# Optimization experiments

Measured on AMD Instinct MI355X. Metric: run time of the kernel, lower is better.

## Reference

```python
import jax, jax.numpy as jnp
import numpy as np

D = 128      # memory_dim
L = 64       # segment_len
SCALE = 1.0 / np.sqrt(D)
LN_EPS = 1e-5


def _layernorm(x, g, b):
    mu = x.mean(-1, keepdims=True)
    var = ((x - mu) ** 2).mean(-1, keepdims=True)
    return (x - mu) * jax.lax.rsqrt(var + LN_EPS) * g + b


def setup_inputs() -> dict:
    key = jax.random.key(0)
    ks = jax.random.split(key, 8)
    B, T, Hd = 4, 4096, 2048
    w = 0.02  # init scale for weight matrices
    return {
        "H": jax.random.normal(ks[0], (B, T, Hd), jnp.float32),
        "M": jax.random.normal(ks[1], (B, D, D), jnp.float32),  # [B,K=128,D=128]
        "ln_g": jnp.ones((Hd,), jnp.float32),
        "ln_b": jnp.zeros((Hd,), jnp.float32),
        "W_eta_w": jax.random.normal(ks[2], (Hd,), jnp.float32) * w,
        "W_eta_b": jnp.full((1,), -5.0, jnp.float32),
        "sum_q": jax.random.normal(ks[3], (D,), jnp.float32),
        "sp_w": jax.random.normal(ks[4], (Hd, D), jnp.float32) * w,
        "sp_b": jnp.zeros((D,), jnp.float32),
        "eta_ch": jnp.ones((D,), jnp.float32),
        "temp": jnp.ones((1,), jnp.float32),
        "W_qkv": jax.random.normal(ks[5], (Hd, 3 * D), jnp.float32) * w,
    }


def reference(H, M, ln_g, ln_b, W_eta_w, W_eta_b, sum_q, sp_w, sp_b, eta_ch, temp, W_qkv):
    B, T, _ = H.shape
    K = M.shape[1]
    S = T // L  # T chosen divisible by segment_len (no-pad branch)

    Hn = _layernorm(H, ln_g, ln_b)                      # [B,T,Hd]

    # ---- write_memory ----
    H_mem = Hn @ sp_w + sp_b                            # [B,T,D]
    eta_tokens = jnp.einsum('bth,h->bt', Hn, W_eta_w) + W_eta_b  # [B,T]

    H_segs = H_mem.reshape(B, S, L, D)
    summary_scores = jnp.einsum('d,bsld->bsl', sum_q, H_segs) * SCALE
    summary_w = jax.nn.softmax(summary_scores, axis=-1)
    Z_seg = jnp.einsum('bsl,bsld->bsd', summary_w, H_segs)       # [B,S,D]

    eta_sig = jax.nn.sigmoid(eta_tokens)                          # [B,T]
    eta_seg = eta_sig.reshape(B, S, L).max(axis=-1)[..., None]    # [B,S,1]

    scores = jnp.einsum('bsd,bkd->bsk', Z_seg, M) * SCALE * jnp.exp(temp)
    A = jax.nn.softmax(scores, axis=-1)                           # [B,S,K]
    DeltaM = jnp.einsum('bsk,bsd->bkd', A, Z_seg * eta_seg)       # [B,K,D]

    eta_avg = eta_seg.mean(axis=1, keepdims=True)                 # [B,1,1]
    gate = eta_avg * jax.nn.sigmoid(eta_ch)                       # [B,1,D]
    M_new = (1.0 - gate) * M + DeltaM / S

    norm_sq = jnp.sum(DeltaM ** 2) / S
    # diversity loss on M_new
    Mn = M_new / jnp.maximum(jnp.linalg.norm(M_new, axis=-1, keepdims=True), 1e-12)
    sim = jnp.einsum('bkd,bjd->bkj', Mn, Mn) * (1.0 - jnp.eye(K, dtype=M.dtype))
    div_loss = jnp.mean(sim ** 2)
    loss = norm_sq * 0.01 + div_loss * 0.1

    # ---- read_memory (from updated memory; K<=1024 -> dense softmax path) ----
    Q_r = Hn @ W_qkv[:, 2 * D:]                                   # [B,T,D]
    r_scores = jnp.einsum('btd,bkd->btk', Q_r, M_new)
    A_r = jax.nn.softmax(r_scores * 2.0, axis=-1)
    C = jnp.einsum('btk,bkd->btd', A_r, M_new)                    # [B,T,D]

    return C, loss
```

## Files before the change

kernel.cpp:

```cpp
#include <hip/hip_runtime.h>
#include <hip/hip_bf16.h>
#include <math.h>

#define HD   2048
#define DD   128
#define TT   4096
#define BB   4
#define MT   (BB*TT)
#define LSEG 64
#define SSEG 64
#define NCOL 256
#define SCALE_D 0.088388347648318447f

typedef _Float16 half8 __attribute__((ext_vector_type(8)));
typedef _Float16 half4v __attribute__((ext_vector_type(4)));
typedef float    f32x4 __attribute__((ext_vector_type(4)));

__device__ __forceinline__ float sigmf(float x){ return 1.f/(1.f+__expf(-x)); }

__device__ __forceinline__ void glds16(const void* g, void* l) {
  __builtin_amdgcn_global_load_lds(
      (const __attribute__((address_space(1))) unsigned int*)g,
      (__attribute__((address_space(3))) unsigned int*)l, 16, 0, 0);
}

__global__ void k_pre(const float* __restrict__ ln_g, const float* __restrict__ ln_b,
                      const float* __restrict__ sp_w, const float* __restrict__ sp_b,
                      const float* __restrict__ W_qkv, const float* __restrict__ W_eta_w,
                      const float* __restrict__ W_eta_b,
                      _Float16* __restrict__ Bp, float* __restrict__ s_vec,
                      float* __restrict__ cb_vec, float* __restrict__ we2,
                      float* __restrict__ scal)
{
  __shared__ float red1[256], red2[256];
  int n = blockIdx.x, t = threadIdx.x;
  float sp = 0.f, cp = 0.f;
  if (n < NCOL) {
    for (int h = t; h < HD; h += 256) {
      float w = (n < DD) ? sp_w[(size_t)h*DD + n] : W_qkv[(size_t)h*384 + 256 + (n-DD)];
      float g = ln_g[h], b = ln_b[h];
      Bp[(size_t)n*HD + h] = (_Float16)(g*w);
      sp += g*w; cp += b*w;
    }
  } else {
    for (int h = t; h < HD; h += 256) {
      float w = W_eta_w[h];
      float g = ln_g[h], b = ln_b[h];
      we2[h] = g*w;
      sp += g*w; cp += b*w;
    }
  }
  red1[t] = sp; red2[t] = cp;
  __syncthreads();
  for (int o = 128; o > 0; o >>= 1) {
    if (t < o) { red1[t] += red1[t+o]; red2[t] += red2[t+o]; }
    __syncthreads();
  }
  if (t == 0) {
    if (n < NCOL) {
      s_vec[n]  = red1[0];
      cb_vec[n] = red2[0] + ((n < DD) ? sp_b[n] : 0.f);
    } else {
      scal[0] = red1[0];
      scal[1] = red2[0] + W_eta_b[0];
      scal[2] = 0.f; scal[3] = 0.f;
    }
  }
}

__launch_bounds__(512, 2)
__global__ void k01(const float* __restrict__ H, const _Float16* __restrict__ Bp,
                    const float* __restrict__ we2,
                    float* __restrict__ Cp, float* __restrict__ Sp)
{
  __shared__ __align__(16) char pool[133120];
  __shared__ float we_s[1024];
  _Float16* sA  = (_Float16*)pool;
  _Float16* sB  = (_Float16*)(pool + 32768);
  float*    sHm = (float*)pool;

  int tid = threadIdx.x;
  int mt = blockIdx.x & 127, kh = blockIdx.x >> 7;
  int m0r = mt * 128;
  int w = tid >> 6, lane = tid & 63;
  int wr = w >> 2, wc = w & 3;
  int fcol = lane & 15, kq = lane >> 4;

  if (tid < 256)
    ((float4*)we_s)[tid] = ((const float4*)(we2 + kh*1024))[tid];
  __syncthreads();

  int r_l = tid >> 2, s4 = tid & 3;
  const float* aptr = H + (size_t)(m0r + r_l)*HD + kh*1024 + s4*16;
  const _Float16* Bph = Bp + kh*1024;
  int bn[4], bsl[4];
#pragma unroll
  for (int i = 0; i < 4; ++i) {
    int idx = i*512 + tid;
    bn[i]  = idx >> 3;
    bsl[i] = (idx & 7) ^ (bn[i] & 7);
  }

  f32x4 acc[4][4];
#pragma unroll
  for (int i = 0; i < 4; ++i)
#pragma unroll
    for (int j = 0; j < 4; ++j) acc[i][j] = (f32x4){0.f,0.f,0.f,0.f};
  float s1 = 0.f, s2 = 0.f, se = 0.f;

  float4 qE0 = *(const float4*)(aptr + 0),  qE1 = *(const float4*)(aptr + 4);
  float4 qE2 = *(const float4*)(aptr + 8),  qE3 = *(const float4*)(aptr + 12);
  __builtin_amdgcn_sched_barrier(0);
#pragma unroll
  for (int i = 0; i < 4; ++i)
    glds16(Bph + (size_t)bn[i]*HD + bsl[i]*8, sB + (size_t)(i*512 + tid)*8);
  __builtin_amdgcn_sched_barrier(0);
  float4 qO0 = *(const float4*)(aptr + 64), qO1 = *(const float4*)(aptr + 68);
  float4 qO2 = *(const float4*)(aptr + 72), qO3 = *(const float4*)(aptr + 76);
  __builtin_amdgcn_sched_barrier(0);
#pragma unroll
  for (int i = 0; i < 4; ++i)
    glds16(Bph + (size_t)bn[i]*HD + 64 + bsl[i]*8,
           sB + 16384 + (size_t)(i*512 + tid)*8);
  __builtin_amdgcn_sched_barrier(0);

#define KSTEP(K0V, SAB, CURB, WB, P0, P1, P2, P3, VMASM, ISSUE)               \
  {                                                                           \
    _Float16* sAc = sA + (SAB)*8192;                                          \
    _Float16* sBc = sB + (CURB)*16384;                                        \
    const int k0 = (K0V);                                                     \
    {                                                                         \
      float v[16] = {P0.x,P0.y,P0.z,P0.w, P1.x,P1.y,P1.z,P1.w,                \
                     P2.x,P2.y,P2.z,P2.w, P3.x,P3.y,P3.z,P3.w};               \
      const float4* wv4 = (const float4*)(we_s + k0 + s4*16);                 \
      float4 u0 = wv4[0], u1 = wv4[1], u2 = wv4[2], u3 = wv4[3];              \
      float uu[16] = {u0.x,u0.y,u0.z,u0.w, u1.x,u1.y,u1.z,u1.w,               \
                      u2.x,u2.y,u2.z,u2.w, u3.x,u3.y,u3.z,u3.w};              \
      half8 h0, h1;                                                           \
      _Pragma("unroll")                                                       \
      for (int jj = 0; jj < 8; ++jj) {                                        \
        s1 += v[jj]; s2 += v[jj]*v[jj]; se += v[jj]*uu[jj];                   \
        h0[jj] = (_Float16)v[jj];                                             \
      }                                                                       \
      _Pragma("unroll")                                                       \
      for (int jj = 8; jj < 16; ++jj) {                                       \
        s1 += v[jj]; s2 += v[jj]*v[jj]; se += v[jj]*uu[jj];                   \
        h1[jj-8] = (_Float16)v[jj];                                           \
      }                                                                       \
      *(half8*)&sAc[r_l*64 + ((s4*2    ) ^ (r_l & 7))*8] = h0;                \
      *(half8*)&sAc[r_l*64 + ((s4*2 + 1) ^ (r_l & 7))*8] = h1;                \
    }                                                                         \
    asm volatile(VMASM ::: "memory");                                         \
    __builtin_amdgcn_s_barrier();                                             \
    __builtin_amdgcn_sched_barrier(0);                                        \
    if (ISSUE) {                                                              \
      _Float16* sBn = sB + (WB)*16384;                                        \
      const _Float16* bsrc = Bph + (k0 + 128);                                \
      _Pragma("unroll")                                                       \
      for (int i = 0; i < 4; ++i)                                             \
        glds16(bsrc + (size_t)bn[i]*HD + bsl[i]*8,                            \
               sBn + (size_t)(i*512 + tid)*8);                                \
      __builtin_amdgcn_sched_barrier(0);                                      \
      const float* ap_ = aptr + k0 + 128;                                     \
      P0 = *(const float4*)(ap_ + 0);  P1 = *(const float4*)(ap_ + 4);        \
      P2 = *(const float4*)(ap_ + 8);  P3 = *(const float4*)(ap_ + 12);       \
      __builtin_amdgcn_sched_barrier(0);                                      \
    }                                                                         \
    __builtin_amdgcn_s_setprio(1);                                            \
    _Pragma("unroll")                                                         \
    for (int ks = 0; ks < 2; ++ks) {                                          \
      half8 af[4], bf[4];                                                     \
      _Pragma("unroll")                                                       \
      for (int rt = 0; rt < 4; ++rt) {                                        \
        int r = wr*64 + rt*16 + fcol;                                         \
        int ch = (ks*4 + kq) ^ (r & 7);                                       \
        af[rt] = *(half8*)&sAc[r*64 + ch*8];                                  \
      }                                                                       \
      _Pragma("unroll")                                                       \
      for (int ct = 0; ct < 4; ++ct) {                                        \
        int n = wc*64 + ct*16 + fcol;                                         \
        int ch = (ks*4 + kq) ^ (n & 7);                                       \
        bf[ct] = *(half8*)&sBc[n*64 + ch*8];                                  \
      }                                                                       \
      _Pragma("unroll")                                                       \
      for (int rt = 0; rt < 4; ++rt)                                          \
        _Pragma("unroll")                                                     \
        for (int ct = 0; ct < 4; ++ct)                                        \
          acc[rt][ct] = __builtin_amdgcn_mfma_f32_16x16x32_f16(af[rt], bf[ct], acc[rt][ct], 0,0,0); \
    }                                                                         \
    __builtin_amdgcn_s_setprio(0);                                            \
  }

#pragma unroll 1
  for (int kp = 0; kp < 2; ++kp) {
    int j0 = kp*384;
    KSTEP(j0,       0, 0, 2, qE0,qE1,qE2,qE3, "s_waitcnt vmcnt(8) lgkmcnt(0)", 1)
    KSTEP(j0 + 64,  1, 1, 0, qO0,qO1,qO2,qO3, "s_waitcnt vmcnt(8) lgkmcnt(0)", 1)
    KSTEP(j0 + 128, 0, 2, 1, qE0,qE1,qE2,qE3, "s_waitcnt vmcnt(8) lgkmcnt(0)", 1)
    KSTEP(j0 + 192, 1, 0, 2, qO0,qO1,qO2,qO3, "s_waitcnt vmcnt(8) lgkmcnt(0)", 1)
    KSTEP(j0 + 256, 0, 1, 0, qE0,qE1,qE2,qE3, "s_waitcnt vmcnt(8) lgkmcnt(0)", 1)
    KSTEP(j0 + 320, 1, 2, 1, qO0,qO1,qO2,qO3, "s_waitcnt vmcnt(8) lgkmcnt(0)", 1)
  }
  KSTEP(768, 0, 0, 2, qE0,qE1,qE2,qE3, "s_waitcnt vmcnt(8) lgkmcnt(0)", 1)
  KSTEP(832, 1, 1, 0, qO0,qO1,qO2,qO3, "s_waitcnt vmcnt(8) lgkmcnt(0)", 1)
  KSTEP(896, 0, 2, 1, qE0,qE1,qE2,qE3, "s_waitcnt vmcnt(8) lgkmcnt(0)", 0)
  KSTEP(960, 1, 0, 2, qO0,qO1,qO2,qO3, "s_waitcnt vmcnt(0) lgkmcnt(0)", 0)
#undef KSTEP

  __syncthreads();

  s1 += __shfl_xor(s1, 1); s1 += __shfl_xor(s1, 2);
  s2 += __shfl_xor(s2, 1); s2 += __shfl_xor(s2, 2);
  se += __shfl_xor(se, 1); se += __shfl_xor(se, 2);
  if (s4 == 0) {
    float4 sv; sv.x = s1; sv.y = s2; sv.z = se; sv.w = 0.f;
    ((float4*)Sp)[(size_t)(kh*128 + mt)*128 + r_l] = sv;
  }

#pragma unroll
  for (int ct = 0; ct < 4; ++ct) {
    int nl = wc*64 + ct*16 + fcol;
#pragma unroll
    for (int rt = 0; rt < 4; ++rt)
#pragma unroll
      for (int r = 0; r < 4; ++r) {
        int m = wr*64 + rt*16 + kq*4 + r;
        sHm[m*260 + nl] = acc[rt][ct][r];
      }
  }
  __syncthreads();

  size_t cbase = (size_t)(kh*128 + mt)*128*256;
#pragma unroll
  for (int j = 0; j < 16; ++j) {
    int idx = j*512 + tid;
    int row = idx >> 6, c4 = (idx & 63)*4;
    *(float4*)&Cp[cbase + (size_t)row*256 + c4] = *(float4*)&sHm[row*260 + c4];
  }
}

__global__ void k_comb(const float* __restrict__ Cp, const float* __restrict__ Sp,
                       const float* __restrict__ s_vec, const float* __restrict__ cb_vec,
                       const float* __restrict__ scal, const float* __restrict__ sum_q,
                       const float* __restrict__ Mmat, const float* __restrict__ temp,
                       float* __restrict__ Q_r, float* __restrict__ Zeta,
                       float* __restrict__ A_seg, float* __restrict__ eta_seg)
{
  __shared__ __align__(16) float sHm[64*132];
  __shared__ float smu_s[64], srs_s[64], seta_s[64];
  __shared__ float sv_s[256], cb_s[256];
  __shared__ float sq_s[128], w64_s[64], Zs[128], red_s[4];
  __shared__ float eta_sh_s;
  int tid = threadIdx.x;
  int seg = blockIdx.x;
  int mt = seg >> 1, half = seg & 1, b = seg >> 6;
  int m0 = seg * 64;
  float scal0 = scal[0], scal1 = scal[1];

  if (tid < 64) {
    float4 a = ((const float4*)Sp)[(size_t)mt*128 + half*64 + tid];
    float4 c = ((const float4*)Sp)[(size_t)(128 + mt)*128 + half*64 + tid];
    float s1 = a.x + c.x, s2 = a.y + c.y, se = a.z + c.z;
    float mu   = s1 * (1.f/HD);
    float var  = s2 * (1.f/HD) - mu*mu;
    float rstd = rsqrtf(var + 1e-5f);
    smu_s[tid] = mu; srs_s[tid] = rstd;
    seta_s[tid] = rstd*(se - mu*scal0) + scal1;
  }
  sv_s[tid] = s_vec[tid];
  cb_s[tid] = cb_vec[tid];
  if (tid < 128) sq_s[tid] = sum_q[tid];
  __syncthreads();

  const float4* c0 = (const float4*)(Cp + ((size_t)mt*128 + half*64)*256);
  const float4* c1 = (const float4*)(Cp + ((size_t)(128 + mt)*128 + half*64)*256);
#pragma unroll
  for (int j = 0; j < 16; ++j) {
    int idx = j*256 + tid;
    int row = idx >> 6, cv = idx & 63;
    float4 v0 = c0[(size_t)row*64 + cv];
    float4 v1 = c1[(size_t)row*64 + cv];
    float mu = smu_s[row], rs = srs_s[row];
    int col = cv*4;
    float4 h;
    h.x = rs*((v0.x+v1.x) - mu*sv_s[col+0]) + cb_s[col+0];
    h.y = rs*((v0.y+v1.y) - mu*sv_s[col+1]) + cb_s[col+1];
    h.z = rs*((v0.z+v1.z) - mu*sv_s[col+2]) + cb_s[col+2];
    h.w = rs*((v0.w+v1.w) - mu*sv_s[col+3]) + cb_s[col+3];
    if (cv < 32) *(float4*)&sHm[row*132 + col] = h;
    else         *(float4*)&Q_r[(size_t)(m0 + row)*DD + (col - 128)] = h;
  }
  __syncthreads();

  int w = tid >> 6, lane = tid & 63;
  if (w == 0) {
    float sc = 0.f;
    const float4* hrow = (const float4*)&sHm[lane*132];
#pragma unroll
    for (int d4 = 0; d4 < 32; ++d4) {
      float4 hv = hrow[d4];
      float4 qv = *(const float4*)&sq_s[d4*4];
      sc += hv.x*qv.x + hv.y*qv.y + hv.z*qv.z + hv.w*qv.w;
    }
    sc *= SCALE_D;
    float mx = sc;
    for (int o = 32; o > 0; o >>= 1) mx = fmaxf(mx, __shfl_xor(mx, o));
    float e = __expf(sc - mx);
    float sm = e;
    for (int o = 32; o > 0; o >>= 1) sm += __shfl_xor(sm, o);
    w64_s[lane] = e / sm;
  } else if (w == 1) {
    float ev = seta_s[lane];
    for (int o = 32; o > 0; o >>= 1) ev = fmaxf(ev, __shfl_xor(ev, o));
    if (lane == 0) { float es = sigmf(ev); eta_sh_s = es; eta_seg[seg] = es; }
  }
  __syncthreads();

  if (tid < 128) {
    float z = 0.f;
    for (int l = 0; l < 64; ++l) z += w64_s[l]*sHm[l*132 + tid];
    Zs[tid] = z;
    Zeta[(size_t)seg*DD + tid] = z * eta_sh_s;
  }
  __syncthreads();

  float sc2 = 0.f;
  if (tid < 128) {
    const float4* mrow = (const float4*)(Mmat + ((size_t)b*DD + tid)*DD);
#pragma unroll
    for (int d4 = 0; d4 < 32; ++d4) {
      float4 mv = mrow[d4];
      sc2 += mv.x*Zs[d4*4] + mv.y*Zs[d4*4+1] + mv.z*Zs[d4*4+2] + mv.w*Zs[d4*4+3];
    }
    sc2 *= SCALE_D * __expf(temp[0]);
    float mx = sc2;
    for (int o = 32; o > 0; o >>= 1) mx = fmaxf(mx, __shfl_xor(mx, o));
    if (lane == 0) red_s[w] = mx;
  }
  __syncthreads();
  float ev2 = 0.f;
  if (tid < 128) {
    float mx = fmaxf(red_s[0], red_s[1]);
    ev2 = __expf(sc2 - mx);
    float sm = ev2;
    for (int o = 32; o > 0; o >>= 1) sm += __shfl_xor(sm, o);
    if (lane == 0) red_s[2 + w] = sm;
  }
  __syncthreads();
  if (tid < 128) {
    float smt = red_s[2] + red_s[3];
    A_seg[(size_t)seg*DD + tid] = ev2 / smt;
  }
}

__global__ void k2b(const float* __restrict__ A_seg, const float* __restrict__ Zeta,
                    const float* __restrict__ eta_seg, const float* __restrict__ Mmat,
                    const float* __restrict__ eta_ch,
                    float* __restrict__ M_new, float* __restrict__ rns_arr,
                    float* __restrict__ scal)
{
  __shared__ float As[64][33];
  __shared__ __align__(16) float Zsl[64*128];
  __shared__ float rowp[32][8];
  __shared__ float eta_av;
  __shared__ float redb[4];
  int tid = threadIdx.x;
  int b = blockIdx.x >> 2, kq = blockIdx.x & 3;
  for (int i = tid; i < 64*32; i += 256) {
    int s = i >> 5, j = i & 31;
    As[s][j] = A_seg[((size_t)b*SSEG + s)*DD + kq*32 + j];
  }
  const float4* z4 = (const float4*)(Zeta + (size_t)b*SSEG*DD);
  float4* zs4 = (float4*)Zsl;
  for (int i = tid; i < 64*32; i += 256) zs4[i] = z4[i];
  if (tid < 64) {
    float ev = eta_seg[(size_t)b*SSEG + tid];
    for (int o=32;o>0;o>>=1) ev += __shfl_xor(ev, o);
    if (tid == 0) eta_av = ev * (1.f/SSEG);
  }
  __syncthreads();
  int kl = tid & 31, dg = tid >> 5;
  int k = kq*32 + kl, d0 = dg*16;
  float dm[16];
#pragma unroll
  for (int j=0;j<16;j++) dm[j]=0.f;
  for (int s = 0; s < 64; ++s) {
    float a = As[s][kl];
    const float* zr = &Zsl[s*128 + d0];
#pragma unroll
    for (int j=0;j<16;j++) dm[j] += a * zr[j];
  }
  float nsq = 0.f;
#pragma unroll
  for (int j=0;j<16;j++) nsq += dm[j]*dm[j];
  float eav = eta_av;
  float mn[16];
  float ss = 0.f;
#pragma unroll
  for (int j=0;j<16;j++) {
    int d = d0 + j;
    float gate = eav * sigmf(eta_ch[d]);
    float v = (1.f - gate)*Mmat[((size_t)b*DD + k)*DD + d] + dm[j]*(1.f/SSEG);
    mn[j] = v; ss += v*v;
  }
#pragma unroll
  for (int j=0;j<16;j+=4) {
    float4 v4; v4.x=mn[j]; v4.y=mn[j+1]; v4.z=mn[j+2]; v4.w=mn[j+3];
    *(float4*)&M_new[((size_t)b*DD + k)*DD + d0 + j] = v4;
  }
  rowp[kl][dg] = ss;
  for (int o=1;o<64;o<<=1) nsq += __shfl_xor(nsq, o);
  if ((tid&63)==0) redb[tid>>6] = nsq;
  __syncthreads();
  if (tid == 0) atomicAdd(&scal[2], redb[0]+redb[1]+redb[2]+redb[3]);
  if (tid < 32) {
    float t2 = 0.f;
#pragma unroll
    for (int g=0; g<8; ++g) t2 += rowp[tid][g];
    float nrm = sqrtf(t2);
    rns_arr[(size_t)b*DD + kq*32 + tid] = 1.f / fmaxf(nrm, 1e-12f);
  }
}

__global__ void k2d(const float* __restrict__ M_new, const float* __restrict__ rns_arr,
                    float* __restrict__ scal)
{
  __shared__ float kr[4][128];
  __shared__ float redb[4];
  int tid = threadIdx.x;
  int b = blockIdx.x >> 5, kq = blockIdx.x & 31;
  for (int i = tid; i < 4*128; i += 256) {
    int ki = i >> 7, d = i & 127;
    kr[ki][d] = M_new[((size_t)b*DD + kq*4 + ki)*DD + d];
  }
  __syncthreads();
  int j = tid & 127, kh = tid >> 7;
  const float* mj = &M_new[((size_t)b*DD + j)*DD];
  float rj = rns_arr[(size_t)b*DD + j];
  float dv = 0.f;
#pragma unroll
  for (int ki2 = 0; ki2 < 2; ++ki2) {
    int kil = kh*2 + ki2;
    int kk = kq*4 + kil;
    float dot = 0.f;
    for (int d = 0; d < 128; d += 4) {
      float4 a = *(const float4*)(mj + d);
      dot += a.x*kr[kil][d] + a.y*kr[kil][d+1] + a.z*kr[kil][d+2] + a.w*kr[kil][d+3];
    }
    if (kk != j) {
      float sv = dot * rj * rns_arr[(size_t)b*DD + kk];
      dv += sv*sv;
    }
  }
  for (int o=1;o<64;o<<=1) dv += __shfl_xor(dv, o);
  if ((tid&63)==0) redb[tid>>6] = dv;
  __syncthreads();
  if (tid==0) atomicAdd(&scal[3], redb[0]+redb[1]+redb[2]+redb[3]);
}

__launch_bounds__(256, 1)
__global__ void k3(const float* __restrict__ Q_r, const float* __restrict__ M_new,
                   const float* __restrict__ scal, float* __restrict__ out)
{
  __shared__ __align__(16) _Float16 Mq[128*132];
  __shared__ __align__(16) _Float16 Mt[128*136];
  __shared__ __align__(16) _Float16 Ps[64*132];
  int tid = threadIdx.x;
  int b = blockIdx.x >> 6, tile = blockIdx.x & 63;
  int t0 = tile*64;
  if (blockIdx.x == 0 && tid == 0) {
    float loss = 0.01f*(scal[2]*(1.f/SSEG)) + 0.1f*(scal[3]*(1.f/(BB*DD*DD)));
    out[(size_t)MT*DD] = loss;
  }
  const float4* m4 = (const float4*)(M_new + (size_t)b*DD*DD);
#pragma unroll
  for (int it = 0; it < 4; ++it) {
    int sb = it*256 + tid;
    int rb = sb & 31, cb = sb >> 5;
    int r0 = rb*4, c0 = cb*4;
    float a[4][4];
#pragma unroll
    for (int j = 0; j < 4; ++j) {
      float4 v = m4[(size_t)(r0+j)*32 + cb];
      a[j][0]=v.x; a[j][1]=v.y; a[j][2]=v.z; a[j][3]=v.w;
    }
#pragma unroll
    for (int j = 0; j < 4; ++j) {
      half4v h; h.x=(_Float16)a[j][0]; h.y=(_Float16)a[j][1];
                h.z=(_Float16)a[j][2]; h.w=(_Float16)a[j][3];
      *(half4v*)&Mq[(r0+j)*132 + c0] = h;
    }
#pragma unroll
    for (int j2 = 0; j2 < 4; ++j2) {
      half4v h; h.x=(_Float16)a[0][j2]; h.y=(_Float16)a[1][j2];
                h.z=(_Float16)a[2][j2]; h.w=(_Float16)a[3][j2];
      *(half4v*)&Mt[(c0+j2)*136 + r0] = h;
    }
  }
  int w = tid >> 6, lane = tid & 63;
  int fcol = lane & 15, kq = lane >> 4;
  int tokA = t0 + w*16 + fcol;
  size_t qbase = ((size_t)b*TT + tokA)*DD;
  half8 af[4];
#pragma unroll
  for (int ks = 0; ks < 4; ++ks) {
    float4 q0 = *(const float4*)&Q_r[qbase + ks*32 + kq*8];
    float4 q1 = *(const float4*)&Q_r[qbase + ks*32 + kq*8 + 4];
    half8 h;
    h[0]=(_Float16)q0.x; h[1]=(_Float16)q0.y; h[2]=(_Float16)q0.z; h[3]=(_Float16)q0.w;
    h[4]=(_Float16)q1.x; h[5]=(_Float16)q1.y; h[6]=(_Float16)q1.z; h[7]=(_Float16)q1.w;
    af[ks] = h;
  }
  __syncthreads();
  f32x4 sacc[8];
#pragma unroll
  for (int nt = 0; nt < 8; ++nt) sacc[nt] = (f32x4){0.f,0.f,0.f,0.f};
#pragma unroll
  for (int nt = 0; nt < 8; ++nt)
#pragma unroll
    for (int ks = 0; ks < 4; ++ks) {
      half8 bf = *(half8*)&Mq[(nt*16 + fcol)*132 + ks*32 + kq*8];
      sacc[nt] = __builtin_amdgcn_mfma_f32_16x16x32_f16(af[ks], bf, sacc[nt], 0,0,0);
    }
#pragma unroll
  for (int nt = 0; nt < 8; ++nt)
#pragma unroll
    for (int r = 0; r < 4; ++r) sacc[nt][r] *= 2.f;
  float mx[4], sm[4];
#pragma unroll
  for (int r = 0; r < 4; ++r) {
    float m = sacc[0][r];
#pragma unroll
    for (int nt = 1; nt < 8; ++nt) m = fmaxf(m, sacc[nt][r]);
#pragma unroll
    for (int o = 1; o < 16; o <<= 1) m = fmaxf(m, __shfl_xor(m, o));
    mx[r] = m;
  }
#pragma unroll
  for (int r = 0; r < 4; ++r) sm[r] = 0.f;
#pragma unroll
  for (int nt = 0; nt < 8; ++nt)
#pragma unroll
    for (int r = 0; r < 4; ++r) {
      float e = __expf(sacc[nt][r] - mx[r]);
      sacc[nt][r] = e; sm[r] += e;
    }
#pragma unroll
  for (int r = 0; r < 4; ++r) {
    float s = sm[r];
#pragma unroll
    for (int o = 1; o < 16; o <<= 1) s += __shfl_xor(s, o);
    sm[r] = 1.f / s;
  }
#pragma unroll
  for (int nt = 0; nt < 8; ++nt)
#pragma unroll
    for (int r = 0; r < 4; ++r) {
      int tk = w*16 + kq*4 + r;
      Ps[tk*132 + nt*16 + fcol] = (_Float16)(sacc[nt][r]*sm[r]);
    }
  __syncthreads();
  half8 pf[4];
#pragma unroll
  for (int ks = 0; ks < 4; ++ks)
    pf[ks] = *(half8*)&Ps[(w*16 + fcol)*132 + ks*32 + kq*8];
  f32x4 cacc[8];
#pragma unroll
  for (int nt = 0; nt < 8; ++nt) cacc[nt] = (f32x4){0.f,0.f,0.f,0.f};
#pragma unroll
  for (int nt = 0; nt < 8; ++nt)
#pragma unroll
    for (int ks = 0; ks < 4; ++ks) {
      half8 bf = *(half8*)&Mt[(nt*16 + fcol)*136 + ks*32 + kq*8];
      cacc[nt] = __builtin_amdgcn_mfma_f32_16x16x32_f16(pf[ks], bf, cacc[nt], 0,0,0);
    }
#pragma unroll
  for (int nt = 0; nt < 8; ++nt)
#pragma unroll
    for (int r = 0; r < 4; ++r) {
      int tk = t0 + w*16 + kq*4 + r;
      out[((size_t)b*TT + tk)*DD + nt*16 + fcol] = cacc[nt][r];
    }
}

extern "C" void kernel_launch(void* const* d_in, const int* in_sizes, int n_in,
                              void* d_out, int out_size, void* d_ws, size_t ws_size,
                              hipStream_t stream)
{
  (void)in_sizes; (void)n_in; (void)out_size; (void)ws_size;
  const float* H       = (const float*)d_in[0];
  const float* Mmat    = (const float*)d_in[1];
  const float* ln_g    = (const float*)d_in[2];
  const float* ln_b    = (const float*)d_in[3];
  const float* W_eta_w = (const float*)d_in[4];
  const float* W_eta_b = (const float*)d_in[5];
  const float* sum_q   = (const float*)d_in[6];
  const float* sp_w    = (const float*)d_in[7];
  const float* sp_b    = (const float*)d_in[8];
  const float* eta_ch  = (const float*)d_in[9];
  const float* temp    = (const float*)d_in[10];
  const float* W_qkv   = (const float*)d_in[11];
  float* out           = (float*)d_out;

  char* wsb = (char*)d_ws;
  size_t off = 0;
  auto alloc = [&](size_t bytes) -> void* {
    void* p = wsb + off;
    off = (off + bytes + 255) & ~(size_t)255;
    return p;
  };
  _Float16* Bp   = (_Float16*)alloc((size_t)NCOL*HD*2);
  float* s_vec   = (float*)alloc(NCOL*4);
  float* cb_vec  = (float*)alloc(NCOL*4);
  float* we2     = (float*)alloc(HD*4);
  float* scal    = (float*)alloc(4*4);
  float* Q_r     = (float*)alloc((size_t)MT*DD*4);
  float* Cp      = (float*)alloc((size_t)2*128*128*256*4);
  float* Sp      = (float*)alloc((size_t)2*128*128*16);
  float* Zeta    = (float*)alloc((size_t)BB*SSEG*DD*4);
  float* A_seg   = (float*)alloc((size_t)BB*SSEG*DD*4);
  float* eta_seg = (float*)alloc((size_t)BB*SSEG*4);
  float* M_new   = (float*)alloc((size_t)BB*DD*DD*4);
  float* rns_arr = (float*)alloc((size_t)BB*DD*4);

  hipLaunchKernelGGL(k_pre, dim3(NCOL+1), dim3(256), 0, stream,
                     ln_g, ln_b, sp_w, sp_b, W_qkv, W_eta_w, W_eta_b,
                     Bp, s_vec, cb_vec, we2, scal);
  hipLaunchKernelGGL(k01, dim3(256), dim3(512), 0, stream,
                     H, Bp, we2, Cp, Sp);
  hipLaunchKernelGGL(k_comb, dim3(BB*SSEG), dim3(256), 0, stream,
                     Cp, Sp, s_vec, cb_vec, scal, sum_q, Mmat, temp,
                     Q_r, Zeta, A_seg, eta_seg);
  hipLaunchKernelGGL(k2b, dim3(16), dim3(256), 0, stream,
                     A_seg, Zeta, eta_seg, Mmat, eta_ch, M_new, rns_arr, scal);
  hipLaunchKernelGGL(k2d, dim3(128), dim3(256), 0, stream,
                     M_new, rns_arr, scal);
  hipLaunchKernelGGL(k3, dim3(256), dim3(256), 0, stream,
                     Q_r, M_new, scal, out);
}
```

Before: 92.40 us.

## Split GEMM K dimension four ways with fp16 partials and smaller LDS tiles

The main GEMM kernel now splits the K=2048 reduction into four 512-wide chunks instead of two, giving 512 blocks with a 32-wide K step and half the LDS footprint, so launch bounds allow more resident blocks per CU. The partial outputs are stored as fp16 rather than fp32, which halves the partial-sum traffic even though there are twice as many partials. The combine kernel reads and sums four fp16 partials and four stat partials per row. This trades more write/read traffic and reduced accuracy in the partials for higher occupancy and parallelism over the H read.

```diff
diff --git a/kernel.cpp b/kernel.cpp
--- a/kernel.cpp
+++ b/kernel.cpp
@@ -68,37 +68,37 @@
   }
 }
 
-__launch_bounds__(512, 2)
+__launch_bounds__(512, 4)
 __global__ void k01(const float* __restrict__ H, const _Float16* __restrict__ Bp,
                     const float* __restrict__ we2,
-                    float* __restrict__ Cp, float* __restrict__ Sp)
+                    _Float16* __restrict__ Cp, float* __restrict__ Sp)
 {
-  __shared__ __align__(16) char pool[133120];
-  __shared__ float we_s[1024];
-  _Float16* sA  = (_Float16*)pool;
-  _Float16* sB  = (_Float16*)(pool + 32768);
-  float*    sHm = (float*)pool;
+  __shared__ __align__(16) char pool[69632];
+  __shared__ float we_s[512];
+  _Float16* sA    = (_Float16*)pool;
+  _Float16* sB    = (_Float16*)(pool + 16384);
+  _Float16* sHm16 = (_Float16*)pool;
 
   int tid = threadIdx.x;
-  int mt = blockIdx.x & 127, kh = blockIdx.x >> 7;
+  int mt = blockIdx.x & 127, khq = blockIdx.x >> 7;
   int m0r = mt * 128;
   int w = tid >> 6, lane = tid & 63;
   int wr = w >> 2, wc = w & 3;
   int fcol = lane & 15, kq = lane >> 4;
 
-  if (tid < 256)
-    ((float4*)we_s)[tid] = ((const float4*)(we2 + kh*1024))[tid];
+  if (tid < 128)
+    ((float4*)we_s)[tid] = ((const float4*)(we2 + khq*512))[tid];
   __syncthreads();
 
   int r_l = tid >> 2, s4 = tid & 3;
-  const float* aptr = H + (size_t)(m0r + r_l)*HD + kh*1024 + s4*16;
-  const _Float16* Bph = Bp + kh*1024;
-  int bn[4], bsl[4];
-#pragma unroll
-  for (int i = 0; i < 4; ++i) {
+  const float* aptr = H + (size_t)(m0r + r_l)*HD + khq*512 + s4*8;
+  const _Float16* Bph = Bp + khq*512;
+  int bn[2], bsl[2];
+#pragma unroll
+  for (int i = 0; i < 2; ++i) {
     int idx = i*512 + tid;
-    bn[i]  = idx >> 3;
-    bsl[i] = (idx & 7) ^ (bn[i] & 7);
+    bn[i]  = idx >> 2;
+    bsl[i] = (idx & 3) ^ (bn[i] & 3);
   }
 
   f32x4 acc[4][4];
@@ -108,79 +108,61 @@
     for (int j = 0; j < 4; ++j) acc[i][j] = (f32x4){0.f,0.f,0.f,0.f};
   float s1 = 0.f, s2 = 0.f, se = 0.f;
 
-  float4 qE0 = *(const float4*)(aptr + 0),  qE1 = *(const float4*)(aptr + 4);
-  float4 qE2 = *(const float4*)(aptr + 8),  qE3 = *(const float4*)(aptr + 12);
+  float4 qE0 = *(const float4*)(aptr + 0), qE1 = *(const float4*)(aptr + 4);
   __builtin_amdgcn_sched_barrier(0);
-#pragma unroll
-  for (int i = 0; i < 4; ++i)
-    glds16(Bph + (size_t)bn[i]*HD + bsl[i]*8, sB + (size_t)(i*512 + tid)*8);
+  glds16(Bph + (size_t)bn[0]*HD + bsl[0]*8, sB + (size_t)tid*8);
+  glds16(Bph + (size_t)bn[1]*HD + bsl[1]*8, sB + (size_t)(512 + tid)*8);
   __builtin_amdgcn_sched_barrier(0);
-  float4 qO0 = *(const float4*)(aptr + 64), qO1 = *(const float4*)(aptr + 68);
-  float4 qO2 = *(const float4*)(aptr + 72), qO3 = *(const float4*)(aptr + 76);
+  float4 qO0 = *(const float4*)(aptr + 32), qO1 = *(const float4*)(aptr + 36);
   __builtin_amdgcn_sched_barrier(0);
-#pragma unroll
-  for (int i = 0; i < 4; ++i)
-    glds16(Bph + (size_t)bn[i]*HD + 64 + bsl[i]*8,
-           sB + 16384 + (size_t)(i*512 + tid)*8);
+  glds16(Bph + (size_t)bn[0]*HD + 32 + bsl[0]*8, sB + 8192 + (size_t)tid*8);
+  glds16(Bph + (size_t)bn[1]*HD + 32 + bsl[1]*8, sB + 8192 + (size_t)(512 + tid)*8);
   __builtin_amdgcn_sched_barrier(0);
 
-#define KSTEP(K0V, SAB, CURB, WB, P0, P1, P2, P3, VMASM, ISSUE)               \
+#define KSTEP(K0V, SAB, CURB, WB, P0, P1, VMASM, ISSUE)                       \
   {                                                                           \
-    _Float16* sAc = sA + (SAB)*8192;                                          \
-    _Float16* sBc = sB + (CURB)*16384;                                        \
+    _Float16* sAc = sA + (SAB)*4096;                                          \
+    _Float16* sBc = sB + (CURB)*8192;                                         \
     const int k0 = (K0V);                                                     \
     {                                                                         \
-      float v[16] = {P0.x,P0.y,P0.z,P0.w, P1.x,P1.y,P1.z,P1.w,                \
-                     P2.x,P2.y,P2.z,P2.w, P3.x,P3.y,P3.z,P3.w};               \
-      const float4* wv4 = (const float4*)(we_s + k0 + s4*16);                 \
-      float4 u0 = wv4[0], u1 = wv4[1], u2 = wv4[2], u3 = wv4[3];              \
-      float uu[16] = {u0.x,u0.y,u0.z,u0.w, u1.x,u1.y,u1.z,u1.w,               \
-                      u2.x,u2.y,u2.z,u2.w, u3.x,u3.y,u3.z,u3.w};              \
-      half8 h0, h1;                                                           \
+      float v[8] = {P0.x,P0.y,P0.z,P0.w, P1.x,P1.y,P1.z,P1.w};                \
+      const float4* wv4 = (const float4*)(we_s + k0 + s4*8);                  \
+      float4 u0 = wv4[0], u1 = wv4[1];                                        \
+      float uu[8] = {u0.x,u0.y,u0.z,u0.w, u1.x,u1.y,u1.z,u1.w};               \
+      half8 h0;                                                               \
       _Pragma("unroll")                                                       \
       for (int jj = 0; jj < 8; ++jj) {                                        \
         s1 += v[jj]; s2 += v[jj]*v[jj]; se += v[jj]*uu[jj];                   \
         h0[jj] = (_Float16)v[jj];                                             \
       }                                                                       \
-      _Pragma("unroll")                                                       \
-      for (int jj = 8; jj < 16; ++jj) {                                       \
-        s1 += v[jj]; s2 += v[jj]*v[jj]; se += v[jj]*uu[jj];                   \
-        h1[jj-8] = (_Float16)v[jj];                                           \
-      }                                                                       \
-      *(half8*)&sAc[r_l*64 + ((s4*2    ) ^ (r_l & 7))*8] = h0;                \
-      *(half8*)&sAc[r_l*64 + ((s4*2 + 1) ^ (r_l & 7))*8] = h1;                \
+      *(half8*)&sAc[r_l*32 + ((s4 ^ (r_l & 3))<<3)] = h0;                     \
     }                                                                         \
     asm volatile(VMASM ::: "memory");                                         \
     __builtin_amdgcn_s_barrier();                                             \
     __builtin_amdgcn_sched_barrier(0);                                        \
     if (ISSUE) {                                                              \
-      _Float16* sBn = sB + (WB)*16384;                                        \
-      const _Float16* bsrc = Bph + (k0 + 128);                                \
-      _Pragma("unroll")                                                       \
-      for (int i = 0; i < 4; ++i)                                             \
-        glds16(bsrc + (size_t)bn[i]*HD + bsl[i]*8,                            \
-               sBn + (size_t)(i*512 + tid)*8);                                \
+      _Float16* sBn = sB + (WB)*8192;                                         \
+      const _Float16* bsrc = Bph + (k0 + 64);                                 \
+      glds16(bsrc + (size_t)bn[0]*HD + bsl[0]*8, sBn + (size_t)tid*8);        \
+      glds16(bsrc + (size_t)bn[1]*HD + bsl[1]*8, sBn + (size_t)(512+tid)*8);  \
       __builtin_amdgcn_sched_barrier(0);                                      \
-      const float* ap_ = aptr + k0 + 128;                                     \
-      P0 = *(const float4*)(ap_ + 0);  P1 = *(const float4*)(ap_ + 4);        \
-      P2 = *(const float4*)(ap_ + 8);  P3 = *(const float4*)(ap_ + 12);       \
+      const float* ap_ = aptr + k0 + 64;                                      \
+      P0 = *(const float4*)(ap_ + 0);                                         \
+      P1 = *(const float4*)(ap_ + 4);                                         \
       __builtin_amdgcn_sched_barrier(0);                                      \
     }                                                                         \
     __builtin_amdgcn_s_setprio(1);                                            \
-    _Pragma("unroll")                                                         \
-    for (int ks = 0; ks < 2; ++ks) {                                          \
+    {                                                                         \
       half8 af[4], bf[4];                                                     \
       _Pragma("unroll")                                                       \
       for (int rt = 0; rt < 4; ++rt) {                                        \
         int r = wr*64 + rt*16 + fcol;                                         \
-        int ch = (ks*4 + kq) ^ (r & 7);                                       \
-        af[rt] = *(half8*)&sAc[r*64 + ch*8];                                  \
+        af[rt] = *(half8*)&sAc[r*32 + ((kq ^ (r & 3))<<3)];                   \
       }                                                                       \
       _Pragma("unroll")                                                       \
       for (int ct = 0; ct < 4; ++ct) {                                        \
         int n = wc*64 + ct*16 + fcol;                                         \
-        int ch = (ks*4 + kq) ^ (n & 7);                                       \
-        bf[ct] = *(half8*)&sBc[n*64 + ch*8];                                  \
+        bf[ct] = *(half8*)&sBc[n*32 + ((kq ^ (n & 3))<<3)];                   \
       }                                                                       \
       _Pragma("unroll")                                                       \
       for (int rt = 0; rt < 4; ++rt)                                          \
@@ -193,18 +175,18 @@
 
 #pragma unroll 1
   for (int kp = 0; kp < 2; ++kp) {
-    int j0 = kp*384;
-    KSTEP(j0,       0, 0, 2, qE0,qE1,qE2,qE3, "s_waitcnt vmcnt(8) lgkmcnt(0)", 1)
-    KSTEP(j0 + 64,  1, 1, 0, qO0,qO1,qO2,qO3, "s_waitcnt vmcnt(8) lgkmcnt(0)", 1)
-    KSTEP(j0 + 128, 0, 2, 1, qE0,qE1,qE2,qE3, "s_waitcnt vmcnt(8) lgkmcnt(0)", 1)
-    KSTEP(j0 + 192, 1, 0, 2, qO0,qO1,qO2,qO3, "s_waitcnt vmcnt(8) lgkmcnt(0)", 1)
-    KSTEP(j0 + 256, 0, 1, 0, qE0,qE1,qE2,qE3, "s_waitcnt vmcnt(8) lgkmcnt(0)", 1)
-    KSTEP(j0 + 320, 1, 2, 1, qO0,qO1,qO2,qO3, "s_waitcnt vmcnt(8) lgkmcnt(0)", 1)
-  }
-  KSTEP(768, 0, 0, 2, qE0,qE1,qE2,qE3, "s_waitcnt vmcnt(8) lgkmcnt(0)", 1)
-  KSTEP(832, 1, 1, 0, qO0,qO1,qO2,qO3, "s_waitcnt vmcnt(8) lgkmcnt(0)", 1)
-  KSTEP(896, 0, 2, 1, qE0,qE1,qE2,qE3, "s_waitcnt vmcnt(8) lgkmcnt(0)", 0)
-  KSTEP(960, 1, 0, 2, qO0,qO1,qO2,qO3, "s_waitcnt vmcnt(0) lgkmcnt(0)", 0)
+    int j0 = kp*192;
+    KSTEP(j0,       0, 0, 2, qE0, qE1, "s_waitcnt vmcnt(4) lgkmcnt(0)", 1)
+    KSTEP(j0 + 32,  1, 1, 0, qO0, qO1, "s_waitcnt vmcnt(4) lgkmcnt(0)", 1)
+    KSTEP(j0 + 64,  0, 2, 1, qE0, qE1, "s_waitcnt vmcnt(4) lgkmcnt(0)", 1)
+    KSTEP(j0 + 96,  1, 0, 2, qO0, qO1, "s_waitcnt vmcnt(4) lgkmcnt(0)", 1)
+    KSTEP(j0 + 128, 0, 1, 0, qE0, qE1, "s_waitcnt vmcnt(4) lgkmcnt(0)", 1)
+    KSTEP(j0 + 160, 1, 2, 1, qO0, qO1, "s_waitcnt vmcnt(4) lgkmcnt(0)", 1)
+  }
+  KSTEP(384, 0, 0, 2, qE0, qE1, "s_waitcnt vmcnt(4) lgkmcnt(0)", 1)
+  KSTEP(416, 1, 1, 0, qO0, qO1, "s_waitcnt vmcnt(4) lgkmcnt(0)", 1)
+  KSTEP(448, 0, 2, 1, qE0, qE1, "s_waitcnt vmcnt(4) lgkmcnt(0)", 0)
+  KSTEP(480, 1, 0, 2, qO0, qO1, "s_waitcnt vmcnt(0) lgkmcnt(0)", 0)
 #undef KSTEP
 
   __syncthreads();
@@ -214,7 +196,7 @@
   se += __shfl_xor(se, 1); se += __shfl_xor(se, 2);
   if (s4 == 0) {
     float4 sv; sv.x = s1; sv.y = s2; sv.z = se; sv.w = 0.f;
-    ((float4*)Sp)[(size_t)(kh*128 + mt)*128 + r_l] = sv;
+    ((float4*)Sp)[(size_t)khq*MT + m0r + r_l] = sv;
   }
 
 #pragma unroll
@@ -225,21 +207,21 @@
 #pragma unroll
       for (int r = 0; r < 4; ++r) {
         int m = wr*64 + rt*16 + kq*4 + r;
-        sHm[m*260 + nl] = acc[rt][ct][r];
+        sHm16[m*264 + nl] = (_Float16)acc[rt][ct][r];
       }
   }
   __syncthreads();
 
-  size_t cbase = (size_t)(kh*128 + mt)*128*256;
-#pragma unroll
-  for (int j = 0; j < 16; ++j) {
+  size_t cbase = (size_t)(khq*128 + mt)*128*256;
+#pragma unroll
+  for (int j = 0; j < 8; ++j) {
     int idx = j*512 + tid;
-    int row = idx >> 6, c4 = (idx & 63)*4;
-    *(float4*)&Cp[cbase + (size_t)row*256 + c4] = *(float4*)&sHm[row*260 + c4];
-  }
-}
-
-__global__ void k_comb(const float* __restrict__ Cp, const float* __restrict__ Sp,
+    int row = idx >> 5, c8 = (idx & 31)*8;
+    *(half8*)&Cp[cbase + (size_t)row*256 + c8] = *(half8*)&sHm16[row*264 + c8];
+  }
+}
+
+__global__ void k_comb(const _Float16* __restrict__ Cp, const float* __restrict__ Sp,
                        const float* __restrict__ s_vec, const float* __restrict__ cb_vec,
                        const float* __restrict__ scal, const float* __restrict__ sum_q,
                        const float* __restrict__ Mmat, const float* __restrict__ temp,
@@ -258,9 +240,13 @@
   float scal0 = scal[0], scal1 = scal[1];
 
   if (tid < 64) {
-    float4 a = ((const float4*)Sp)[(size_t)mt*128 + half*64 + tid];
-    float4 c = ((const float4*)Sp)[(size_t)(128 + mt)*128 + half*64 + tid];
-    float s1 = a.x + c.x, s2 = a.y + c.y, se = a.z + c.z;
+    int gr = m0 + tid;
+    float s1 = 0.f, s2 = 0.f, se = 0.f;
+#pragma unroll
+    for (int kh = 0; kh < 4; ++kh) {
+      float4 a = ((const float4*)Sp)[(size_t)kh*MT + gr];
+      s1 += a.x; s2 += a.y; se += a.z;
+    }
     float mu   = s1 * (1.f/HD);
     float var  = s2 * (1.f/HD) - mu*mu;
     float rstd = rsqrtf(var + 1e-5f);
@@ -272,23 +258,36 @@
   if (tid < 128) sq_s[tid] = sum_q[tid];
   __syncthreads();
 
-  const float4* c0 = (const float4*)(Cp + ((size_t)mt*128 + half*64)*256);
-  const float4* c1 = (const float4*)(Cp + ((size_t)(128 + mt)*128 + half*64)*256);
-#pragma unroll
-  for (int j = 0; j < 16; ++j) {
+  const _Float16* cb0 = Cp + ((size_t)(0*128 + mt)*128 + half*64)*256;
+  const _Float16* cb1 = Cp + ((size_t)(1*128 + mt)*128 + half*64)*256;
+  const _Float16* cb2 = Cp + ((size_t)(2*128 + mt)*128 + half*64)*256;
+  const _Float16* cb3 = Cp + ((size_t)(3*128 + mt)*128 + half*64)*256;
+#pragma unroll
+  for (int j = 0; j < 8; ++j) {
     int idx = j*256 + tid;
-    int row = idx >> 6, cv = idx & 63;
-    float4 v0 = c0[(size_t)row*64 + cv];
-    float4 v1 = c1[(size_t)row*64 + cv];
+    int row = idx >> 5, c8 = (idx & 31)*8;
+    size_t off = (size_t)row*256 + c8;
+    half8 a0 = *(const half8*)&cb0[off];
+    half8 a1 = *(const half8*)&cb1[off];
+    half8 a2 = *(const half8*)&cb2[off];
+    half8 a3 = *(const half8*)&cb3[off];
     float mu = smu_s[row], rs = srs_s[row];
-    int col = cv*4;
-    float4 h;
-    h.x = rs*((v0.x+v1.x) - mu*sv_s[col+0]) + cb_s[col+0];
-    h.y = rs*((v0.y+v1.y) - mu*sv_s[col+1]) + cb_s[col+1];
-    h.z = rs*((v0.z+v1.z) - mu*sv_s[col+2]) + cb_s[col+2];
-    h.w = rs*((v0.w+v1.w) - mu*sv_s[col+3]) + cb_s[col+3];
-    if (cv < 32) *(float4*)&sHm[row*132 + col] = h;
-    else         *(float4*)&Q_r[(size_t)(m0 + row)*DD + (col - 128)] = h;
+    float hv[8];
+#pragma unroll
+    for (int e = 0; e < 8; ++e) {
+      float s = ((float)a0[e] + (float)a1[e]) + ((float)a2[e] + (float)a3[e]);
+      int col = c8 + e;
+      hv[e] = rs*(s - mu*sv_s[col]) + cb_s[col];
+    }
+    float4 v0; v0.x=hv[0]; v0.y=hv[1]; v0.z=hv[2]; v0.w=hv[3];
+    float4 v1; v1.x=hv[4]; v1.y=hv[5]; v1.z=hv[6]; v1.w=hv[7];
+    if (c8 < 128) {
+      *(float4*)&sHm[row*132 + c8]     = v0;
+      *(float4*)&sHm[row*132 + c8 + 4] = v1;
+    } else {
+      *(float4*)&Q_r[(size_t)(m0 + row)*DD + c8 - 128] = v0;
+      *(float4*)&Q_r[(size_t)(m0 + row)*DD + c8 - 124] = v1;
+    }
   }
   __syncthreads();
 
@@ -615,8 +614,8 @@
   float* we2     = (float*)alloc(HD*4);
   float* scal    = (float*)alloc(4*4);
   float* Q_r     = (float*)alloc((size_t)MT*DD*4);
-  float* Cp      = (float*)alloc((size_t)2*128*128*256*4);
-  float* Sp      = (float*)alloc((size_t)2*128*128*16);
+  _Float16* Cp   = (_Float16*)alloc((size_t)4*128*128*256*2);
+  float* Sp      = (float*)alloc((size_t)4*MT*16);
   float* Zeta    = (float*)alloc((size_t)BB*SSEG*DD*4);
   float* A_seg   = (float*)alloc((size_t)BB*SSEG*DD*4);
   float* eta_seg = (float*)alloc((size_t)BB*SSEG*4);
@@ -626,7 +625,7 @@
   hipLaunchKernelGGL(k_pre, dim3(NCOL+1), dim3(256), 0, stream,
                      ln_g, ln_b, sp_w, sp_b, W_qkv, W_eta_w, W_eta_b,
                      Bp, s_vec, cb_vec, we2, scal);
-  hipLaunchKernelGGL(k01, dim3(256), dim3(512), 0, stream,
+  hipLaunchKernelGGL(k01, dim3(512), dim3(512), 0, stream,
                      H, Bp, we2, Cp, Sp);
   hipLaunchKernelGGL(k_comb, dim3(BB*SSEG), dim3(256), 0, stream,
                      Cp, Sp, s_vec, cb_vec, scal, sum_q, Mmat, temp,
```

New measurement: 245.6 us. 2.66x slower.
